# Kernel optimization log

Measured on AMD Instinct MI355X. Metric: run time of the kernel, lower is better.

Reference implementation:

```python
import jax, jax.numpy as jnp
import numpy as np
from jax import lax

USER_NUM = 60000
ITEM_NUM = 40000
N_NODES = USER_NUM + ITEM_NUM
EMB = 64
NNZ = 3200000
N_LAYERS = 3
ALPHA = 0.1


def setup_inputs() -> dict:
    key = jax.random.key(0)
    k1, k2, k3, k4, k5 = jax.random.split(key, 5)
    rows = jax.random.randint(k1, (NNZ,), 0, N_NODES, dtype=jnp.int32)
    cols = jax.random.randint(k2, (NNZ,), 0, N_NODES, dtype=jnp.int32)
    # normalized adjacency values are small positives
    vals = jax.random.uniform(k3, (NNZ,), dtype=jnp.float32) * 0.05
    user_emb = jax.random.normal(k4, (USER_NUM, EMB), dtype=jnp.float32) * 0.1
    item_emb = jax.random.normal(k5, (ITEM_NUM, EMB), dtype=jnp.float32) * 0.1
    return {"rows": rows, "cols": cols, "vals": vals,
            "user_emb": user_emb, "item_emb": item_emb}


def reference(rows, cols, vals, user_emb, item_emb):
    # ego = cat(user, item); e_out starts at zeros (first forward call).
    ego = jnp.concatenate([user_emb, item_emb], axis=0)  # [N, d]
    e0 = jnp.zeros_like(ego)

    def step(e, _):
        # torch.sparse.mm(A, e.clone().detach()) -> SpMM with stop_gradient,
        # matching the original's detach of the propagated state.
        gathered = vals[:, None] * lax.stop_gradient(e)[cols]  # [nnz, d]
        msg = jax.ops.segment_sum(gathered, rows, num_segments=N_NODES)
        e_new = (1.0 - ALPHA) * msg + ego
        return e_new, None

    e_out, _ = lax.scan(step, e0, None, length=N_LAYERS)
    return e_out[:USER_NUM], e_out[USER_NUM:]
```

## Files before the change

kernel.cpp:

```cpp
#include <hip/hip_runtime.h>
#include <hip/hip_fp16.h>


#define USER_NUM 60000
#define ITEM_NUM 40000
#define N_NODES  100000
#define EMB      64
#define NNZ      3200000
#define OMA      0.9f
#define BR       128
#define NB       782
#define TILE     4096
#define CAPB     4480

typedef float f32x4 __attribute__((ext_vector_type(4)));

__global__ __launch_bounds__(256) void conv_init(const float* __restrict__ ue,
                                                 const float* __restrict__ ie,
                                                 __half* __restrict__ dst,
                                                 int* __restrict__ bcursor) {
    int t = blockIdx.x * 256 + threadIdx.x;
    if (t < NB) bcursor[t] = t * CAPB;
    const int total8 = N_NODES * EMB / 8;
    if (t >= total8) return;
    size_t f0 = (size_t)t * 8;
    const size_t usz = (size_t)USER_NUM * EMB;
    const float4* s4 = (f0 < usz) ? (const float4*)(ue + f0)
                                  : (const float4*)(ie + (f0 - usz));
    float4 x = s4[0], y = s4[1];
    union { float4 f4; __half2 h2[4]; } o;
    o.h2[0] = __floats2half2_rn(x.x, x.y);
    o.h2[1] = __floats2half2_rn(x.z, x.w);
    o.h2[2] = __floats2half2_rn(y.x, y.y);
    o.h2[3] = __floats2half2_rn(y.z, y.w);
    ((float4*)dst)[t] = o.f4;
}

__global__ __launch_bounds__(512) void bucket_scatter(const int* __restrict__ rows,
                                                      const int* __restrict__ cols,
                                                      const float* __restrict__ vals,
                                                      int* __restrict__ bcursor,
                                                      int2* __restrict__ ebuf) {
    __shared__ int bins[NB + 1];
    __shared__ int lcur[NB];
    __shared__ int wsum[8];
    __shared__ int2 stage[TILE];
    int t = threadIdx.x;
    int lane = t & 63, w = t >> 6;
    for (int b = t; b <= NB; b += 512) bins[b] = 0;
    __syncthreads();

    int e0 = blockIdx.x * TILE;
    int mybk[8], mypk[8];
    float myv[8];
#pragma unroll
    for (int j = 0; j < 8; ++j) {
        int i = e0 + t + 512 * j;
        mybk[j] = -1;
        if (i < NNZ) {
            int r = rows[i], c = cols[i];
            myv[j]  = vals[i] * OMA;
            mybk[j] = r >> 7;
            mypk[j] = c | ((r & 127) << 17);
            atomicAdd(&bins[mybk[j]], 1);
        }
    }
    __syncthreads();

    int b0 = t * 2;
    int r0 = (b0     < NB) ? bins[b0]     : 0;
    int r1 = (b0 + 1 < NB) ? bins[b0 + 1] : 0;
    int s = r0 + r1;
    int incl = s;
#pragma unroll
    for (int off = 1; off < 64; off <<= 1) {
        int v = __shfl_up(incl, off, 64);
        if (lane >= off) incl += v;
    }
    if (lane == 63) wsum[w] = incl;
    __syncthreads();
    int prefix = 0;
#pragma unroll
    for (int i = 0; i < 8; ++i) if (i < w) prefix += wsum[i];
    int excl = prefix + incl - s;
    if (b0     < NB) { bins[b0]     = excl; lcur[b0]     = excl; excl += r0; }
    if (b0 + 1 < NB) { bins[b0 + 1] = excl; lcur[b0 + 1] = excl; excl += r1; }
    if (t == 511) bins[NB] = prefix + incl;
    __syncthreads();

#pragma unroll
    for (int j = 0; j < 8; ++j) {
        if (mybk[j] >= 0) {
            int p = atomicAdd(&lcur[mybk[j]], 1);
            stage[p] = make_int2(mypk[j], __float_as_int(myv[j]));
        }
    }
    __syncthreads();

    for (int b = t; b < NB; b += 512) {
        int st = bins[b], en = bins[b + 1];
        int cnt = en - st;
        if (cnt > 0) lcur[b] = atomicAdd(&bcursor[b], cnt) - st;
    }
    __syncthreads();

    int total = bins[NB];
    for (int i = t; i < total; i += 512) {
        int lo = 0, hi = NB;
        while (hi - lo > 1) {
            int mid = (lo + hi) >> 1;
            if (bins[mid] <= i) lo = mid; else hi = mid;
        }
        ebuf[(size_t)(lcur[lo] + i)] = stage[i];
    }
}

__global__ __launch_bounds__(512) void sort_spmm1(const int* __restrict__ bcursor,
                                                  int2* __restrict__ ebuf,
                                                  int* __restrict__ row_start,
                                                  int* __restrict__ row_end,
                                                  const __half* __restrict__ ego_h,
                                                  const float* __restrict__ ue,
                                                  const float* __restrict__ ie,
                                                  __half* __restrict__ e2h) {
    __shared__ int2 stage[CAPB];
    __shared__ int rhist[BR], rofs[BR], rcur[BR];
    int bk = blockIdx.x, t = threadIdx.x;
    int s = bk * CAPB;
    int cnt = min(bcursor[bk] - s, CAPB);

    if (t < BR) rhist[t] = 0;
    __syncthreads();
    for (int i = t; i < cnt; i += 512) {
        int2 v = ebuf[(size_t)(s + i)];
        stage[i] = v;
        atomicAdd(&rhist[(v.x >> 17) & 127], 1);
    }
    __syncthreads();
    if (t < 64) {
        int h0 = rhist[2 * t], h1 = rhist[2 * t + 1];
        int pair = h0 + h1;
        int incl = pair;
#pragma unroll
        for (int off = 1; off < 64; off <<= 1) {
            int v = __shfl_up(incl, off, 64);
            if (t >= off) incl += v;
        }
        int base = incl - pair;
        rofs[2 * t]     = base;      rcur[2 * t]     = base;
        rofs[2 * t + 1] = base + h0; rcur[2 * t + 1] = base + h0;
    }
    __syncthreads();
    if (t < BR) {
        int r = (bk << 7) + t;
        if (r < N_NODES) {
            row_start[r] = s + rofs[t];
            row_end[r]   = s + rofs[t] + rhist[t];
        }
    }
    for (int i = t; i < cnt; i += 512) {
        int2 v = stage[i];
        int p = atomicAdd(&rcur[(v.x >> 17) & 127], 1);
        ebuf[(size_t)(s + p)] = v;
    }
    __syncthreads();

    int lane  = t & 15;
    int qbase = (t & 63) & ~15;
    int g = t >> 4;
    const float2* srcv = (const float2*)ego_h;
#pragma unroll
    for (int rr = 0; rr < 4; ++rr) {
        int rl = (g << 2) | rr;
        int r  = (bk << 7) + rl;
        if (r >= N_NODES) break;
        const float* egop = (r < USER_NUM) ? (ue + (size_t)r * EMB)
                                           : (ie + (size_t)(r - USER_NUM) * EMB);
        float4 acc = ((const float4*)egop)[lane];
        int ss = s + rofs[rl];
        int ee = ss + rhist[rl];
        int2 cv = (ss + lane < ee) ? ebuf[(size_t)(ss + lane)] : make_int2(0, 0);
        for (int k = ss; k < ee; k += 16) {
            int idxn = k + 16 + lane;
            int2 nv = (idxn < ee) ? ebuf[(size_t)idxn] : make_int2(0, 0);
#pragma unroll
            for (int j = 0; j < 16; ++j) {
                int   cj = __shfl(cv.x, qbase + j, 64) & 0x1FFFF;
                float vj = __int_as_float(__shfl(cv.y, qbase + j, 64));
                union { float2 f2; __half2 h2[2]; } u;
                u.f2 = srcv[(size_t)cj * 16 + lane];
                float2 a = __half22float2(u.h2[0]);
                float2 b = __half22float2(u.h2[1]);
                acc.x += vj * a.x; acc.y += vj * a.y;
                acc.z += vj * b.x; acc.w += vj * b.y;
            }
            cv = nv;
        }
        union { float2 f2; __half2 h2[2]; } o;
        o.h2[0] = __floats2half2_rn(acc.x, acc.y);
        o.h2[1] = __floats2half2_rn(acc.z, acc.w);
        ((float2*)e2h)[(size_t)r * 16 + lane] = o.f2;
    }
}

__global__ __launch_bounds__(256) void spmm2(const int* __restrict__ row_start,
                                             const int* __restrict__ row_end,
                                             const int2* __restrict__ colval,
                                             const __half* __restrict__ src,
                                             const float* __restrict__ ue,
                                             const float* __restrict__ ie,
                                             float* __restrict__ outb) {
    int tid = blockIdx.x * 256 + threadIdx.x;
    int r = tid >> 4;
    if (r >= N_NODES) return;
    int lane  = threadIdx.x & 15;
    int qbase = (threadIdx.x & 63) & ~15;

    const float* egop = (r < USER_NUM) ? (ue + (size_t)r * EMB)
                                       : (ie + (size_t)(r - USER_NUM) * EMB);
    float4 acc = ((const float4*)egop)[lane];
    const float2* srcv = (const float2*)src;
    int s = row_start[r], e = row_end[r];

    int2 cv = (s + lane < e) ? colval[(size_t)(s + lane)] : make_int2(0, 0);
    for (int k = s; k < e; k += 16) {
        int idxn = k + 16 + lane;
        int2 nv = (idxn < e) ? colval[(size_t)idxn] : make_int2(0, 0);
#pragma unroll
        for (int j = 0; j < 16; ++j) {
            int   cj = __shfl(cv.x, qbase + j, 64) & 0x1FFFF;
            float vj = __int_as_float(__shfl(cv.y, qbase + j, 64));
            union { float2 f2; __half2 h2[2]; } u;
            u.f2 = srcv[(size_t)cj * 16 + lane];
            float2 a = __half22float2(u.h2[0]);
            float2 b = __half22float2(u.h2[1]);
            acc.x += vj * a.x; acc.y += vj * a.y;
            acc.z += vj * b.x; acc.w += vj * b.y;
        }
        cv = nv;
    }
    f32x4 av = { acc.x, acc.y, acc.z, acc.w };
    __builtin_nontemporal_store(av, &((f32x4*)outb)[(size_t)r * 16 + lane]);
}

extern "C" void kernel_launch(void* const* d_in, const int* in_sizes, int n_in,
                              void* d_out, int out_size, void* d_ws, size_t ws_size,
                              hipStream_t stream) {
    const int*   rows = (const int*)d_in[0];
    const int*   cols = (const int*)d_in[1];
    const float* vals = (const float*)d_in[2];
    const float* ue   = (const float*)d_in[3];
    const float* ie   = (const float*)d_in[4];
    float* out = (float*)d_out;

    char* ws = (char*)d_ws;
    __half* ego_h    = (__half*)ws;
    __half* e2h      = (__half*)(ws + 12800000);
    int2*   ebuf     = (int2*)(ws + 25600000);
    int*    row_s    = (int*)(ws + 53626880);
    int*    row_e    = (int*)(ws + 54026880);
    int*    bcursor  = (int*)(ws + 54426880);

    const int convBlocks = (N_NODES * EMB / 8 + 255) / 256;
    conv_init<<<convBlocks, 256, 0, stream>>>(ue, ie, ego_h, bcursor);

    const int tiles = (NNZ + TILE - 1) / TILE;
    bucket_scatter<<<tiles, 512, 0, stream>>>(rows, cols, vals, bcursor, ebuf);
    sort_spmm1<<<NB, 512, 0, stream>>>(bcursor, ebuf, row_s, row_e, ego_h, ue, ie, e2h);

    const int spmmBlocks = (N_NODES * 16 + 255) / 256;
    spmm2<<<spmmBlocks, 256, 0, stream>>>(row_s, row_e, ebuf, e2h, ue, ie, out);
}
```

Baseline: 274.7 us.

## Sort edges by source-column segment within row buckets for gather locality

Within each 128-row bucket, edges are now binned by (column segment of 16K nodes, local row), so all rows in a block gather from one column range at a time. This is meant to improve L2 locality of the random half-precision source gathers. The second SpMM becomes one 512-thread block per bucket and reads the saved bin offsets, and its edge loads use nontemporal hints. The cost is a larger shared-memory histogram and scan, per-bin variable-length inner loops in place of the fixed 16-step unrolled loop with prefetch, and more branch divergence.

```diff
diff --git a/kernel.cpp b/kernel.cpp
--- a/kernel.cpp
+++ b/kernel.cpp
@@ -7,11 +7,15 @@
 #define N_NODES  100000
 #define EMB      64
 #define NNZ      3200000
-#define OMA      0.9f
+#define OMA       0.9f
 #define BR       128
 #define NB       782
 #define TILE     4096
 #define CAPB     4480
+#define SEG_SHIFT 14
+#define NSEG     7
+#define NBIN     896
+#define RG       904
 
 typedef float f32x4 __attribute__((ext_vector_type(4)));
 
@@ -84,7 +88,7 @@
     for (int i = 0; i < 8; ++i) if (i < w) prefix += wsum[i];
     int excl = prefix + incl - s;
     if (b0     < NB) { bins[b0]     = excl; lcur[b0]     = excl; excl += r0; }
-    if (b0 + 1 < NB) { bins[b0 + 1] = excl; lcur[b0 + 1] = excl; excl += r1; }
+    if (b0 + 1 < NB) { bins[b0 + 1] = excl; lcur[b0 + 1] = excl; }
     if (t == 511) bins[NB] = prefix + incl;
     __syncthreads();
 
@@ -117,130 +121,167 @@
 
 __global__ __launch_bounds__(512) void sort_spmm1(const int* __restrict__ bcursor,
                                                   int2* __restrict__ ebuf,
-                                                  int* __restrict__ row_start,
-                                                  int* __restrict__ row_end,
+                                                  int* __restrict__ rofs_g,
                                                   const __half* __restrict__ ego_h,
                                                   const float* __restrict__ ue,
                                                   const float* __restrict__ ie,
                                                   __half* __restrict__ e2h) {
     __shared__ int2 stage[CAPB];
-    __shared__ int rhist[BR], rofs[BR], rcur[BR];
+    __shared__ int rhist[NBIN], rofs[NBIN + 1], rcur[NBIN];
+    __shared__ int wsum[8];
     int bk = blockIdx.x, t = threadIdx.x;
+    int lane64 = t & 63, w = t >> 6;
     int s = bk * CAPB;
     int cnt = min(bcursor[bk] - s, CAPB);
 
-    if (t < BR) rhist[t] = 0;
+    for (int i = t; i < NBIN; i += 512) rhist[i] = 0;
     __syncthreads();
     for (int i = t; i < cnt; i += 512) {
         int2 v = ebuf[(size_t)(s + i)];
         stage[i] = v;
-        atomicAdd(&rhist[(v.x >> 17) & 127], 1);
-    }
-    __syncthreads();
-    if (t < 64) {
-        int h0 = rhist[2 * t], h1 = rhist[2 * t + 1];
-        int pair = h0 + h1;
-        int incl = pair;
-#pragma unroll
-        for (int off = 1; off < 64; off <<= 1) {
-            int v = __shfl_up(incl, off, 64);
-            if (t >= off) incl += v;
-        }
-        int base = incl - pair;
-        rofs[2 * t]     = base;      rcur[2 * t]     = base;
-        rofs[2 * t + 1] = base + h0; rcur[2 * t + 1] = base + h0;
-    }
-    __syncthreads();
-    if (t < BR) {
-        int r = (bk << 7) + t;
-        if (r < N_NODES) {
-            row_start[r] = s + rofs[t];
-            row_end[r]   = s + rofs[t] + rhist[t];
-        }
-    }
+        int bin = (((v.x & 0x1FFFF) >> SEG_SHIFT) << 7) | (v.x >> 17);
+        atomicAdd(&rhist[bin], 1);
+    }
+    __syncthreads();
+    int b0 = t * 2;
+    int h0 = (b0     < NBIN) ? rhist[b0]     : 0;
+    int h1 = (b0 + 1 < NBIN) ? rhist[b0 + 1] : 0;
+    int sum = h0 + h1;
+    int incl = sum;
+#pragma unroll
+    for (int off = 1; off < 64; off <<= 1) {
+        int v = __shfl_up(incl, off, 64);
+        if (lane64 >= off) incl += v;
+    }
+    if (lane64 == 63) wsum[w] = incl;
+    __syncthreads();
+    int prefix = 0;
+#pragma unroll
+    for (int i = 0; i < 8; ++i) if (i < w) prefix += wsum[i];
+    int excl = prefix + incl - sum;
+    if (b0     < NBIN) { rofs[b0]     = excl; rcur[b0]     = excl; excl += h0; }
+    if (b0 + 1 < NBIN) { rofs[b0 + 1] = excl; rcur[b0 + 1] = excl; }
+    if (t == 0) rofs[NBIN] = cnt;
+    __syncthreads();
+
     for (int i = t; i < cnt; i += 512) {
         int2 v = stage[i];
-        int p = atomicAdd(&rcur[(v.x >> 17) & 127], 1);
+        int bin = (((v.x & 0x1FFFF) >> SEG_SHIFT) << 7) | (v.x >> 17);
+        int p = atomicAdd(&rcur[bin], 1);
         ebuf[(size_t)(s + p)] = v;
     }
+    for (int i = t; i <= NBIN; i += 512) rofs_g[bk * RG + i] = rofs[i];
     __syncthreads();
 
     int lane  = t & 15;
     int qbase = (t & 63) & ~15;
-    int g = t >> 4;
+    int rlb   = (t >> 4) << 2;
     const float2* srcv = (const float2*)ego_h;
+    float4 acc[4];
 #pragma unroll
     for (int rr = 0; rr < 4; ++rr) {
-        int rl = (g << 2) | rr;
-        int r  = (bk << 7) + rl;
-        if (r >= N_NODES) break;
-        const float* egop = (r < USER_NUM) ? (ue + (size_t)r * EMB)
-                                           : (ie + (size_t)(r - USER_NUM) * EMB);
-        float4 acc = ((const float4*)egop)[lane];
-        int ss = s + rofs[rl];
-        int ee = ss + rhist[rl];
-        int2 cv = (ss + lane < ee) ? ebuf[(size_t)(ss + lane)] : make_int2(0, 0);
-        for (int k = ss; k < ee; k += 16) {
-            int idxn = k + 16 + lane;
-            int2 nv = (idxn < ee) ? ebuf[(size_t)idxn] : make_int2(0, 0);
-#pragma unroll
-            for (int j = 0; j < 16; ++j) {
-                int   cj = __shfl(cv.x, qbase + j, 64) & 0x1FFFF;
-                float vj = __int_as_float(__shfl(cv.y, qbase + j, 64));
-                union { float2 f2; __half2 h2[2]; } u;
-                u.f2 = srcv[(size_t)cj * 16 + lane];
-                float2 a = __half22float2(u.h2[0]);
-                float2 b = __half22float2(u.h2[1]);
-                acc.x += vj * a.x; acc.y += vj * a.y;
-                acc.z += vj * b.x; acc.w += vj * b.y;
+        int r = (bk << 7) + rlb + rr;
+        acc[rr] = make_float4(0.f, 0.f, 0.f, 0.f);
+        if (r < N_NODES) {
+            const float* egop = (r < USER_NUM) ? (ue + (size_t)r * EMB)
+                                               : (ie + (size_t)(r - USER_NUM) * EMB);
+            acc[rr] = ((const float4*)egop)[lane];
+        }
+    }
+    for (int seg = 0; seg < NSEG; ++seg) {
+#pragma unroll
+        for (int rr = 0; rr < 4; ++rr) {
+            int bin = (seg << 7) | (rlb + rr);
+            int ss = s + rofs[bin];
+            int ee = s + rofs[bin + 1];
+            for (int k = ss; k < ee; k += 16) {
+                int rem = ee - k; if (rem > 16) rem = 16;
+                int2 cv = (lane < rem) ? ebuf[(size_t)(k + lane)] : make_int2(0, 0);
+                for (int j = 0; j < rem; ++j) {
+                    int   cj = __shfl(cv.x, qbase + j, 64) & 0x1FFFF;
+                    float vj = __int_as_float(__shfl(cv.y, qbase + j, 64));
+                    union { float2 f2; __half2 h2[2]; } u;
+                    u.f2 = srcv[(size_t)cj * 16 + lane];
+                    float2 a = __half22float2(u.h2[0]);
+                    float2 b = __half22float2(u.h2[1]);
+                    acc[rr].x += vj * a.x; acc[rr].y += vj * a.y;
+                    acc[rr].z += vj * b.x; acc[rr].w += vj * b.y;
+                }
             }
-            cv = nv;
-        }
-        union { float2 f2; __half2 h2[2]; } o;
-        o.h2[0] = __floats2half2_rn(acc.x, acc.y);
-        o.h2[1] = __floats2half2_rn(acc.z, acc.w);
-        ((float2*)e2h)[(size_t)r * 16 + lane] = o.f2;
-    }
-}
-
-__global__ __launch_bounds__(256) void spmm2(const int* __restrict__ row_start,
-                                             const int* __restrict__ row_end,
-                                             const int2* __restrict__ colval,
+        }
+    }
+#pragma unroll
+    for (int rr = 0; rr < 4; ++rr) {
+        int r = (bk << 7) + rlb + rr;
+        if (r < N_NODES) {
+            union { float2 f2; __half2 h2[2]; } o;
+            o.h2[0] = __floats2half2_rn(acc[rr].x, acc[rr].y);
+            o.h2[1] = __floats2half2_rn(acc[rr].z, acc[rr].w);
+            ((float2*)e2h)[(size_t)r * 16 + lane] = o.f2;
+        }
+    }
+}
+
+__global__ __launch_bounds__(512) void spmm2(const int* __restrict__ rofs_g,
+                                             const int2* __restrict__ ebuf,
                                              const __half* __restrict__ src,
                                              const float* __restrict__ ue,
                                              const float* __restrict__ ie,
                                              float* __restrict__ outb) {
-    int tid = blockIdx.x * 256 + threadIdx.x;
-    int r = tid >> 4;
-    if (r >= N_NODES) return;
-    int lane  = threadIdx.x & 15;
-    int qbase = (threadIdx.x & 63) & ~15;
-
-    const float* egop = (r < USER_NUM) ? (ue + (size_t)r * EMB)
-                                       : (ie + (size_t)(r - USER_NUM) * EMB);
-    float4 acc = ((const float4*)egop)[lane];
+    __shared__ int rofs[NBIN + 1];
+    int bk = blockIdx.x, t = threadIdx.x;
+    for (int i = t; i <= NBIN; i += 512) rofs[i] = rofs_g[bk * RG + i];
+    __syncthreads();
+    int s = bk * CAPB;
+    int lane  = t & 15;
+    int qbase = (t & 63) & ~15;
+    int rlb   = (t >> 4) << 2;
     const float2* srcv = (const float2*)src;
-    int s = row_start[r], e = row_end[r];
-
-    int2 cv = (s + lane < e) ? colval[(size_t)(s + lane)] : make_int2(0, 0);
-    for (int k = s; k < e; k += 16) {
-        int idxn = k + 16 + lane;
-        int2 nv = (idxn < e) ? colval[(size_t)idxn] : make_int2(0, 0);
-#pragma unroll
-        for (int j = 0; j < 16; ++j) {
-            int   cj = __shfl(cv.x, qbase + j, 64) & 0x1FFFF;
-            float vj = __int_as_float(__shfl(cv.y, qbase + j, 64));
-            union { float2 f2; __half2 h2[2]; } u;
-            u.f2 = srcv[(size_t)cj * 16 + lane];
-            float2 a = __half22float2(u.h2[0]);
-            float2 b = __half22float2(u.h2[1]);
-            acc.x += vj * a.x; acc.y += vj * a.y;
-            acc.z += vj * b.x; acc.w += vj * b.y;
-        }
-        cv = nv;
-    }
-    f32x4 av = { acc.x, acc.y, acc.z, acc.w };
-    __builtin_nontemporal_store(av, &((f32x4*)outb)[(size_t)r * 16 + lane]);
+    const unsigned long long* eb8 = (const unsigned long long*)ebuf;
+    float4 acc[4];
+#pragma unroll
+    for (int rr = 0; rr < 4; ++rr) {
+        int r = (bk << 7) + rlb + rr;
+        acc[rr] = make_float4(0.f, 0.f, 0.f, 0.f);
+        if (r < N_NODES) {
+            const float* egop = (r < USER_NUM) ? (ue + (size_t)r * EMB)
+                                               : (ie + (size_t)(r - USER_NUM) * EMB);
+            acc[rr] = ((const float4*)egop)[lane];
+        }
+    }
+    for (int seg = 0; seg < NSEG; ++seg) {
+#pragma unroll
+        for (int rr = 0; rr < 4; ++rr) {
+            int bin = (seg << 7) | (rlb + rr);
+            int ss = s + rofs[bin];
+            int ee = s + rofs[bin + 1];
+            for (int k = ss; k < ee; k += 16) {
+                int rem = ee - k; if (rem > 16) rem = 16;
+                unsigned long long pv = 0;
+                if (lane < rem) pv = __builtin_nontemporal_load(&eb8[(size_t)(k + lane)]);
+                int cx = (int)(pv & 0xFFFFFFFFull);
+                int cy = (int)(pv >> 32);
+                for (int j = 0; j < rem; ++j) {
+                    int   cj = __shfl(cx, qbase + j, 64) & 0x1FFFF;
+                    float vj = __int_as_float(__shfl(cy, qbase + j, 64));
+                    union { float2 f2; __half2 h2[2]; } u;
+                    u.f2 = srcv[(size_t)cj * 16 + lane];
+                    float2 a = __half22float2(u.h2[0]);
+                    float2 b = __half22float2(u.h2[1]);
+                    acc[rr].x += vj * a.x; acc[rr].y += vj * a.y;
+                    acc[rr].z += vj * b.x; acc[rr].w += vj * b.y;
+                }
+            }
+        }
+    }
+#pragma unroll
+    for (int rr = 0; rr < 4; ++rr) {
+        int r = (bk << 7) + rlb + rr;
+        if (r < N_NODES) {
+            f32x4 av = { acc[rr].x, acc[rr].y, acc[rr].z, acc[rr].w };
+            __builtin_nontemporal_store(av, &((f32x4*)outb)[(size_t)r * 16 + lane]);
+        }
+    }
 }
 
 extern "C" void kernel_launch(void* const* d_in, const int* in_sizes, int n_in,
@@ -257,17 +298,14 @@
     __half* ego_h    = (__half*)ws;
     __half* e2h      = (__half*)(ws + 12800000);
     int2*   ebuf     = (int2*)(ws + 25600000);
-    int*    row_s    = (int*)(ws + 53626880);
-    int*    row_e    = (int*)(ws + 54026880);
-    int*    bcursor  = (int*)(ws + 54426880);
+    int*    rofs_g   = (int*)(ws + 53626880);
+    int*    bcursor  = (int*)(ws + 56454592);
 
     const int convBlocks = (N_NODES * EMB / 8 + 255) / 256;
     conv_init<<<convBlocks, 256, 0, stream>>>(ue, ie, ego_h, bcursor);
 
     const int tiles = (NNZ + TILE - 1) / TILE;
     bucket_scatter<<<tiles, 512, 0, stream>>>(rows, cols, vals, bcursor, ebuf);
-    sort_spmm1<<<NB, 512, 0, stream>>>(bcursor, ebuf, row_s, row_e, ego_h, ue, ie, e2h);
-
-    const int spmmBlocks = (N_NODES * 16 + 255) / 256;
-    spmm2<<<spmmBlocks, 256, 0, stream>>>(row_s, row_e, ebuf, e2h, ue, ie, out);
-}
+    sort_spmm1<<<NB, 512, 0, stream>>>(bcursor, ebuf, rofs_g, ego_h, ue, ie, e2h);
+    spmm2<<<NB, 512, 0, stream>>>(rofs_g, ebuf, e2h, ue, ie, out);
+}
```

Measured after the change: 423.0 us. 54.0% more time.
